# Kernel optimization log

Measured on AMD Instinct MI355X. Metric: run time of the kernel, lower is better.

Reference implementation:

```python
import jax, jax.numpy as jnp
import numpy as np

DIM = 384
HEADS = 6
HIDDEN = int(DIM * 4.0)
EPS = 1e-6

def setup_inputs() -> dict:
    key = jax.random.key(0)
    ks = jax.random.split(key, 8)
    s = 0.02
    return {
        "x": jax.random.normal(ks[0], (4, 2048, DIM), dtype=jnp.float32),
        "w_qkv": jax.random.normal(ks[1], (DIM, 3 * DIM), dtype=jnp.float32) * s,
        "b_qkv": jnp.zeros((3 * DIM,), dtype=jnp.float32),
        "w_proj": jax.random.normal(ks[2], (DIM, DIM), dtype=jnp.float32) * s,
        "b_proj": jnp.zeros((DIM,), dtype=jnp.float32),
        "w_fc1": jax.random.normal(ks[3], (DIM, HIDDEN), dtype=jnp.float32) * s,
        "b_fc1": jnp.zeros((HIDDEN,), dtype=jnp.float32),
        "w_fc2": jax.random.normal(ks[4], (HIDDEN, DIM), dtype=jnp.float32) * s,
        "b_fc2": jnp.zeros((DIM,), dtype=jnp.float32),
        "g1": jnp.ones((DIM,), dtype=jnp.float32),
        "beta1": jnp.zeros((DIM,), dtype=jnp.float32),
        "g2": jnp.ones((DIM,), dtype=jnp.float32),
        "beta2": jnp.zeros((DIM,), dtype=jnp.float32),
    }

def _layernorm(x, g, b):
    mu = jnp.mean(x, axis=-1, keepdims=True)
    var = jnp.mean(jnp.square(x - mu), axis=-1, keepdims=True)
    return (x - mu) * jax.lax.rsqrt(var + EPS) * g + b

def _attention(x, w_qkv, b_qkv, w_proj, b_proj):
    B, N, C = x.shape
    H = HEADS
    Dh = C // H
    qkv = x @ w_qkv + b_qkv                      # [B,N,3C]
    qkv = qkv.reshape(B, N, 3, H, Dh)
    q = jnp.transpose(qkv[:, :, 0], (0, 2, 1, 3))  # [B,H,N,Dh]
    k = jnp.transpose(qkv[:, :, 1], (0, 2, 1, 3))
    v = jnp.transpose(qkv[:, :, 2], (0, 2, 1, 3))
    scale = Dh ** -0.5
    attn = jnp.einsum('bhnd,bhmd->bhnm', q, k) * scale
    attn = jax.nn.softmax(attn, axis=-1)
    out = jnp.einsum('bhnm,bhmd->bhnd', attn, v)
    out = jnp.transpose(out, (0, 2, 1, 3)).reshape(B, N, C)
    return out @ w_proj + b_proj

def _mlp(x, w_fc1, b_fc1, w_fc2, b_fc2):
    h = jax.nn.gelu(x @ w_fc1 + b_fc1, approximate=False)
    return h @ w_fc2 + b_fc2

def reference(x, w_qkv, b_qkv, w_proj, b_proj, w_fc1, b_fc1, w_fc2, b_fc2, g1, beta1, g2, beta2):
    x = x + _attention(_layernorm(x, g1, beta1), w_qkv, b_qkv, w_proj, b_proj)
    x = x + _mlp(_layernorm(x, g2, beta2), w_fc1, b_fc1, w_fc2, b_fc2)
    return x
```

## Files before the change

### kernel.cpp

```cpp
#include <hip/hip_runtime.h>
#include <hip/hip_bf16.h>

#define TOK 8192
#define CDIM 384
#define HEADS 6
#define DH 64
#define HID 1536
#define SEQ 2048

#define QSCALE 0.18033688011112042f

typedef short bf16x8 __attribute__((ext_vector_type(8)));
typedef short bf16x4 __attribute__((ext_vector_type(4)));
typedef float f32x4 __attribute__((ext_vector_type(4)));
typedef void __attribute__((address_space(1))) GV;
typedef void __attribute__((address_space(3))) SV;

__device__ __forceinline__ short f2bf(float f) {
    __hip_bfloat16 h = __float2bfloat16(f);
    return *reinterpret_cast<short*>(&h);
}

__device__ __forceinline__ int pack_bf2(float a, float b) {
    __hip_bfloat162 h2 = __float22bfloat162_rn(make_float2(a, b));
    int r;
    __builtin_memcpy(&r, &h2, 4);
    return r;
}

__device__ __forceinline__ void gl_lds16(const short* g, short* lds) {
    __builtin_amdgcn_global_load_lds((GV*)g, (SV*)lds, 16, 0, 0);
}

__device__ __forceinline__ float gelu_exact(float v) {
    return 0.5f * v * (1.0f + erff(v * 0.70710678118654752f));
}

#define SWZ4(r) ((((r) & 3) ^ (((r) >> 2) & 3)))

__global__ __launch_bounds__(128) void ln_kernel(const float* __restrict__ x,
                                                 const float* __restrict__ g,
                                                 const float* __restrict__ bta,
                                                 short* __restrict__ y) {
    const int row = blockIdx.x;
    const float* xr = x + (size_t)row * CDIM;
    const int t = threadIdx.x;
    float v0 = xr[t], v1 = xr[t + 128], v2 = xr[t + 256];
    float s = v0 + v1 + v2;
    float ss = v0 * v0 + v1 * v1 + v2 * v2;
#pragma unroll
    for (int off = 1; off < 64; off <<= 1) {
        s += __shfl_xor(s, off);
        ss += __shfl_xor(ss, off);
    }
    __shared__ float sh[4];
    const int wv = t >> 6;
    if ((t & 63) == 0) { sh[wv] = s; sh[2 + wv] = ss; }
    __syncthreads();
    s = sh[0] + sh[1];
    ss = sh[2] + sh[3];
    const float mu = s * (1.0f / CDIM);
    const float var = ss * (1.0f / CDIM) - mu * mu;
    const float rs = rsqrtf(var + 1e-6f);
    short* yr = y + (size_t)row * CDIM;
    yr[t]       = f2bf((v0 - mu) * rs * g[t]       + bta[t]);
    yr[t + 128] = f2bf((v1 - mu) * rs * g[t + 128] + bta[t + 128]);
    yr[t + 256] = f2bf((v2 - mu) * rs * g[t + 256] + bta[t + 256]);
}

__global__ __launch_bounds__(256) void transpose_bf16(const float* __restrict__ w,
                                                      short* __restrict__ wT,
                                                      int K, int N) {
    __shared__ float t[32][33];
    const int bx = blockIdx.x * 32, by = blockIdx.y * 32;
    const int tx = threadIdx.x & 31, ty = threadIdx.x >> 5;
#pragma unroll
    for (int i = 0; i < 4; ++i)
        t[ty + i * 8][tx] = w[(size_t)(by + ty + i * 8) * N + bx + tx];
    __syncthreads();
#pragma unroll
    for (int i = 0; i < 4; ++i)
        wT[(size_t)(bx + ty + i * 8) * K + by + tx] = f2bf(t[tx][ty + i * 8]);
}

template <int MODE, int MT>
__global__ __launch_bounds__(256) void mfma_gemm(const short* __restrict__ A,
                                                 const short* __restrict__ WT,
                                                 const float* __restrict__ bias,
                                                 const float* __restrict__ resid,
                                                 float* __restrict__ outF,
                                                 short* __restrict__ outB,
                                                 short* __restrict__ qb,
                                                 short* __restrict__ kb,
                                                 short* __restrict__ vtb,
                                                 int M, int N, int K) {
    constexpr int BN = (MT == 4) ? 128 : 64;
    __shared__ __align__(16) short As[128 * 32];
    __shared__ __align__(16) short Bs[BN * 32];

    const int tid  = threadIdx.x;
    const int w    = tid >> 6;
    const int lane = tid & 63;
    const int quad = lane >> 4;
    const int n15  = lane & 15;
    const int wr   = (MT == 4) ? (w >> 1) : w;
    const int wc   = (MT == 4) ? (w & 1) : 0;
    const int m0   = blockIdx.y * 128;
    const int n0   = blockIdx.x * BN;

    f32x4 acc[MT][4];
#pragma unroll
    for (int i = 0; i < MT; ++i)
#pragma unroll
        for (int j = 0; j < 4; ++j) {
            acc[i][j][0] = 0; acc[i][j][1] = 0; acc[i][j][2] = 0; acc[i][j][3] = 0;
        }

    const int ca0 = tid, ca1 = tid + 256;
    const int swz = SWZ4(n15);

    for (int k0 = 0; k0 < K; k0 += 32) {
        __syncthreads();
        gl_lds16(A  + (size_t)(m0 + (ca0 >> 2)) * K + k0 + (((ca0 & 3) ^ SWZ4(ca0 >> 2)) * 8), As + w * 512);
        gl_lds16(A  + (size_t)(m0 + (ca1 >> 2)) * K + k0 + (((ca1 & 3) ^ SWZ4(ca1 >> 2)) * 8), As + 2048 + w * 512);
        gl_lds16(WT + (size_t)(n0 + (ca0 >> 2)) * K + k0 + (((ca0 & 3) ^ SWZ4(ca0 >> 2)) * 8), Bs + w * 512);
        if (MT == 4)
            gl_lds16(WT + (size_t)(n0 + (ca1 >> 2)) * K + k0 + (((ca1 & 3) ^ SWZ4(ca1 >> 2)) * 8), Bs + 2048 + w * 512);
        __syncthreads();

        bf16x8 af[MT], bfr[4];
#pragma unroll
        for (int mt = 0; mt < MT; ++mt)
            af[mt] = *(const bf16x8*)&As[(wr * (MT * 16) + mt * 16 + n15) * 32 + ((quad ^ swz) * 8)];
#pragma unroll
        for (int nt = 0; nt < 4; ++nt)
            bfr[nt] = *(const bf16x8*)&Bs[(wc * 64 + nt * 16 + n15) * 32 + ((quad ^ swz) * 8)];
#pragma unroll
        for (int mt = 0; mt < MT; ++mt)
#pragma unroll
            for (int nt = 0; nt < 4; ++nt)
                acc[mt][nt] = __builtin_amdgcn_mfma_f32_16x16x32_bf16(af[mt], bfr[nt], acc[mt][nt], 0, 0, 0);
    }

#pragma unroll
    for (int nt = 0; nt < 4; ++nt) {
        const int col = n0 + wc * 64 + nt * 16 + n15;
        const float bv = bias[col];
        if constexpr (MODE == 2) {
            const int part = col / CDIM;
            const int rem  = col - part * CDIM;
            const int h    = rem >> 6;
            const int d    = rem & 63;
#pragma unroll
            for (int mt = 0; mt < MT; ++mt)
#pragma unroll
                for (int rr = 0; rr < 4; ++rr) {
                    const int r  = m0 + wr * (MT * 16) + mt * 16 + quad * 4 + rr;
                    const int bi = r >> 11;
                    const int n  = r & 2047;
                    float o = acc[mt][nt][rr] + bv;
                    if (part == 0) o *= QSCALE;
                    const short v = f2bf(o);
                    if (part == 0)
                        qb[((size_t)(bi * HEADS + h) * SEQ + n) * DH + d] = v;
                    else if (part == 1)
                        kb[((size_t)(bi * HEADS + h) * SEQ + n) * DH + d] = v;
                    else
                        vtb[((size_t)(bi * HEADS + h) * DH + d) * SEQ + n] = v;
                }
        } else {
#pragma unroll
            for (int mt = 0; mt < MT; ++mt)
#pragma unroll
                for (int rr = 0; rr < 4; ++rr) {
                    const int r = m0 + wr * (MT * 16) + mt * 16 + quad * 4 + rr;
                    float o = acc[mt][nt][rr] + bv;
                    if constexpr (MODE == 1) {
                        outB[(size_t)r * N + col] = f2bf(gelu_exact(o));
                    } else {
                        if (resid) o += resid[(size_t)r * N + col];
                        outF[(size_t)r * N + col] = o;
                    }
                }
        }
    }
}

__global__ __launch_bounds__(256) void attn_mfma(const short* __restrict__ qb,
                                                 const short* __restrict__ kb,
                                                 const short* __restrict__ vtb,
                                                 short* __restrict__ outp) {
    __shared__ __align__(16) short Ql[64 * 64];
    __shared__ __align__(16) short Kl[64 * 64];
    __shared__ __align__(16) short Vtl[64 * 64];

    const int qt = blockIdx.x;
    const int bh = blockIdx.z * HEADS + blockIdx.y;

    const int tid  = threadIdx.x;
    const int w    = tid >> 6;
    const int lane = tid & 63;
    const int quad = lane >> 4;
    const int n15  = lane & 15;
    const int swz  = n15 & 7;

    const size_t headoff = (size_t)bh * SEQ * DH;

    {
        const short* qg = qb + headoff + (size_t)qt * 64 * DH;
#pragma unroll
        for (int i = 0; i < 2; ++i) {
            const int c = (w * 2 + i) * 64 + lane;
            const int r = c >> 3, p = c & 7;
            gl_lds16(qg + r * 64 + ((p ^ (r & 7)) * 8), Ql + (c - lane) * 8);
        }
    }

    const short* kptr[2];
    const short* vptr[2];
#pragma unroll
    for (int i = 0; i < 2; ++i) {
        const int c = (w * 2 + i) * 64 + lane;
        const int r = c >> 3, p = c & 7;
        kptr[i] = kb + headoff + r * 64 + ((p ^ (r & 7)) * 8);
        vptr[i] = vtb + (size_t)bh * DH * SEQ + (size_t)r * SEQ + ((p ^ (r & 7)) * 8);
    }

    f32x4 O[4];
    float lacc = 0.0f;
#pragma unroll
    for (int nt = 0; nt < 4; ++nt) { O[nt][0] = 0; O[nt][1] = 0; O[nt][2] = 0; O[nt][3] = 0; }

    bf16x8 qf[2];

    for (int kt = 0; kt < SEQ / 64; ++kt) {
        __syncthreads();
#pragma unroll
        for (int i = 0; i < 2; ++i) {
            gl_lds16(kptr[i], Kl + ((w * 2 + i) * 64) * 8);
            gl_lds16(vptr[i], Vtl + ((w * 2 + i) * 64) * 8);
            kptr[i] += 64 * DH;
            vptr[i] += 64;
        }
        __syncthreads();

        if (kt == 0) {
            qf[0] = *(const bf16x8*)&Ql[(w * 16 + n15) * 64 + ((quad ^ swz) * 8)];
            qf[1] = *(const bf16x8*)&Ql[(w * 16 + n15) * 64 + (((4 + quad) ^ swz) * 8)];
        }

        f32x4 S[4];
#pragma unroll
        for (int nt = 0; nt < 4; ++nt) {
            S[nt][0] = 0; S[nt][1] = 0; S[nt][2] = 0; S[nt][3] = 0;
#pragma unroll
            for (int kc = 0; kc < 2; ++kc) {
                const bf16x8 kf = *(const bf16x8*)&Kl[(nt * 16 + n15) * 64 + (((kc * 4 + quad) ^ swz) * 8)];
                S[nt] = __builtin_amdgcn_mfma_f32_16x16x32_bf16(kf, qf[kc], S[nt], 0, 0, 0);
            }
        }

        bf16x4 af16[4];
#pragma unroll
        for (int nt = 0; nt < 4; ++nt) {
            float p0 = exp2f(S[nt][0]), p1 = exp2f(S[nt][1]);
            float p2 = exp2f(S[nt][2]), p3 = exp2f(S[nt][3]);
            lacc += (p0 + p1) + (p2 + p3);
            int pk[2];
            pk[0] = pack_bf2(p0, p1);
            pk[1] = pack_bf2(p2, p3);
            __builtin_memcpy(&af16[nt], pk, 8);
        }

#pragma unroll
        for (int kc16 = 0; kc16 < 4; ++kc16) {
#pragma unroll
            for (int ntd = 0; ntd < 4; ++ntd) {
                const int row = ntd * 16 + n15;
                const int pchunk = (2 * kc16 + (quad >> 1)) ^ swz;
                const bf16x4 vf = *(const bf16x4*)&Vtl[row * 64 + pchunk * 8 + (quad & 1) * 4];
                O[ntd] = __builtin_amdgcn_mfma_f32_16x16x16bf16_1k(af16[kc16], vf, O[ntd], 0, 0, 0);
            }
        }
    }

    lacc += __shfl_xor(lacc, 16);
    lacc += __shfl_xor(lacc, 32);
    const float invq = 1.0f / lacc;
#pragma unroll
    for (int rr = 0; rr < 4; ++rr) {
        const float inv = __shfl(invq, quad * 4 + rr);
        const int row = qt * 64 + w * 16 + quad * 4 + rr;
#pragma unroll
        for (int nt = 0; nt < 4; ++nt)
            outp[(size_t)(blockIdx.z * SEQ + row) * CDIM + blockIdx.y * DH + nt * 16 + n15] =
                f2bf(O[nt][rr] * inv);
    }
}

extern "C" void kernel_launch(void* const* d_in, const int* in_sizes, int n_in,
                              void* d_out, int out_size, void* d_ws, size_t ws_size,
                              hipStream_t stream) {
    const float* x      = (const float*)d_in[0];
    const float* w_qkv  = (const float*)d_in[1];
    const float* b_qkv  = (const float*)d_in[2];
    const float* w_proj = (const float*)d_in[3];
    const float* b_proj = (const float*)d_in[4];
    const float* w_fc1  = (const float*)d_in[5];
    const float* b_fc1  = (const float*)d_in[6];
    const float* w_fc2  = (const float*)d_in[7];
    const float* b_fc2  = (const float*)d_in[8];
    const float* g1     = (const float*)d_in[9];
    const float* beta1  = (const float*)d_in[10];
    const float* g2     = (const float*)d_in[11];
    const float* beta2  = (const float*)d_in[12];
    float* out = (float*)d_out;

    short* qkvT = (short*)d_ws;
    short* projT = qkvT + 1152 * 384;
    short* fc1T  = projT + 384 * 384;
    short* fc2T  = fc1T + 1536 * 384;
    short* y     = fc2T + 384 * 1536;
    short* qb    = y + (size_t)TOK * 384;
    short* kb    = qb + (size_t)TOK * 384;
    short* vtb   = kb + (size_t)TOK * 384;
    short* attn  = vtb + (size_t)TOK * 384;
    short* hbuf  = attn + (size_t)TOK * 384;

    transpose_bf16<<<dim3(1152 / 32, 384 / 32), 256, 0, stream>>>(w_qkv, qkvT, CDIM, 3 * CDIM);
    transpose_bf16<<<dim3(384 / 32, 384 / 32), 256, 0, stream>>>(w_proj, projT, CDIM, CDIM);
    transpose_bf16<<<dim3(1536 / 32, 384 / 32), 256, 0, stream>>>(w_fc1, fc1T, CDIM, HID);
    transpose_bf16<<<dim3(384 / 32, 1536 / 32), 256, 0, stream>>>(w_fc2, fc2T, HID, CDIM);

    ln_kernel<<<TOK, 128, 0, stream>>>(x, g1, beta1, y);
    mfma_gemm<2, 4><<<dim3(1152 / 128, TOK / 128), 256, 0, stream>>>(
        y, qkvT, b_qkv, nullptr, nullptr, nullptr, qb, kb, vtb, TOK, 3 * CDIM, CDIM);
    attn_mfma<<<dim3(SEQ / 64, HEADS, 4), 256, 0, stream>>>(qb, kb, vtb, attn);
    mfma_gemm<0, 2><<<dim3(CDIM / 64, TOK / 128), 256, 0, stream>>>(
        attn, projT, b_proj, x, out, nullptr, nullptr, nullptr, nullptr, TOK, CDIM, CDIM);
    ln_kernel<<<TOK, 128, 0, stream>>>(out, g2, beta2, y);
    mfma_gemm<1, 4><<<dim3(HID / 128, TOK / 128), 256, 0, stream>>>(
        y, fc1T, b_fc1, nullptr, nullptr, hbuf, nullptr, nullptr, nullptr, TOK, HID, CDIM);
    mfma_gemm<0, 2><<<dim3(CDIM / 64, TOK / 128), 256, 0, stream>>>(
        hbuf, fc2T, b_fc2, out, out, nullptr, nullptr, nullptr, nullptr, TOK, CDIM, HID);
}
```

Baseline: 275.9 us.

## Double GEMM K-tile to 64 with 8-way swizzle, merge weight transposes, vectorize V stores

The MFMA GEMM now stages 64-wide K tiles in LDS instead of 32, with an XOR swizzle over 8 chunks. This halves the number of barrier pairs per K loop and issues more MFMAs per sync, at the cost of doubled LDS use per block. The four weight-transpose launches are merged into a single kernel that selects the matrix from the block index, saving launch overhead. The QKV epilogue writes the transposed V as packed short4 stores and hoists index math out of the per-row loop.

Result: faster. 255.5 us (-7.4%).

```diff
diff --git a/kernel.cpp b/kernel.cpp
--- a/kernel.cpp
+++ b/kernel.cpp
@@ -35,8 +35,6 @@
 __device__ __forceinline__ float gelu_exact(float v) {
     return 0.5f * v * (1.0f + erff(v * 0.70710678118654752f));
 }
-
-#define SWZ4(r) ((((r) & 3) ^ (((r) >> 2) & 3)))
 
 __global__ __launch_bounds__(128) void ln_kernel(const float* __restrict__ x,
                                                  const float* __restrict__ g,
@@ -68,11 +66,22 @@
     yr[t + 256] = f2bf((v2 - mu) * rs * g[t + 256] + bta[t + 256]);
 }
 
-__global__ __launch_bounds__(256) void transpose_bf16(const float* __restrict__ w,
-                                                      short* __restrict__ wT,
-                                                      int K, int N) {
+__global__ __launch_bounds__(256) void transpose_all(const float* __restrict__ w_qkv,
+                                                     const float* __restrict__ w_proj,
+                                                     const float* __restrict__ w_fc1,
+                                                     const float* __restrict__ w_fc2,
+                                                     short* __restrict__ qkvT,
+                                                     short* __restrict__ projT,
+                                                     short* __restrict__ fc1T,
+                                                     short* __restrict__ fc2T) {
+    int b = blockIdx.x;
+    const float* w; short* o; int K, N, nb;
+    if (b < 432)       { w = w_qkv;  o = qkvT;  K = 384;  N = 1152; nb = 36; }
+    else if (b < 576)  { b -= 432;  w = w_proj; o = projT; K = 384;  N = 384;  nb = 12; }
+    else if (b < 1152) { b -= 576;  w = w_fc1;  o = fc1T;  K = 384;  N = 1536; nb = 48; }
+    else               { b -= 1152; w = w_fc2;  o = fc2T;  K = 1536; N = 384;  nb = 12; }
+    const int bx = (b % nb) * 32, by = (b / nb) * 32;
     __shared__ float t[32][33];
-    const int bx = blockIdx.x * 32, by = blockIdx.y * 32;
     const int tx = threadIdx.x & 31, ty = threadIdx.x >> 5;
 #pragma unroll
     for (int i = 0; i < 4; ++i)
@@ -80,7 +89,7 @@
     __syncthreads();
 #pragma unroll
     for (int i = 0; i < 4; ++i)
-        wT[(size_t)(bx + ty + i * 8) * K + by + tx] = f2bf(t[tx][ty + i * 8]);
+        o[(size_t)(bx + ty + i * 8) * K + by + tx] = f2bf(t[tx][ty + i * 8]);
 }
 
 template <int MODE, int MT>
@@ -95,8 +104,8 @@
                                                  short* __restrict__ vtb,
                                                  int M, int N, int K) {
     constexpr int BN = (MT == 4) ? 128 : 64;
-    __shared__ __align__(16) short As[128 * 32];
-    __shared__ __align__(16) short Bs[BN * 32];
+    __shared__ __align__(16) short As[128 * 64];
+    __shared__ __align__(16) short Bs[BN * 64];
 
     const int tid  = threadIdx.x;
     const int w    = tid >> 6;
@@ -107,6 +116,7 @@
     const int wc   = (MT == 4) ? (w & 1) : 0;
     const int m0   = blockIdx.y * 128;
     const int n0   = blockIdx.x * BN;
+    const int swz  = n15 & 7;
 
     f32x4 acc[MT][4];
 #pragma unroll
@@ -116,30 +126,41 @@
             acc[i][j][0] = 0; acc[i][j][1] = 0; acc[i][j][2] = 0; acc[i][j][3] = 0;
         }
 
-    const int ca0 = tid, ca1 = tid + 256;
-    const int swz = SWZ4(n15);
-
-    for (int k0 = 0; k0 < K; k0 += 32) {
+    for (int k0 = 0; k0 < K; k0 += 64) {
         __syncthreads();
-        gl_lds16(A  + (size_t)(m0 + (ca0 >> 2)) * K + k0 + (((ca0 & 3) ^ SWZ4(ca0 >> 2)) * 8), As + w * 512);
-        gl_lds16(A  + (size_t)(m0 + (ca1 >> 2)) * K + k0 + (((ca1 & 3) ^ SWZ4(ca1 >> 2)) * 8), As + 2048 + w * 512);
-        gl_lds16(WT + (size_t)(n0 + (ca0 >> 2)) * K + k0 + (((ca0 & 3) ^ SWZ4(ca0 >> 2)) * 8), Bs + w * 512);
-        if (MT == 4)
-            gl_lds16(WT + (size_t)(n0 + (ca1 >> 2)) * K + k0 + (((ca1 & 3) ^ SWZ4(ca1 >> 2)) * 8), Bs + 2048 + w * 512);
+#pragma unroll
+        for (int i = 0; i < 4; ++i) {
+            const int c = i * 256 + tid;
+            const int r = c >> 3, p = c & 7;
+            gl_lds16(A + (size_t)(m0 + r) * K + k0 + ((p ^ (r & 7)) * 8),
+                     As + (i * 256 + w * 64) * 8);
+        }
+#pragma unroll
+        for (int i = 0; i < BN / 32; ++i) {
+            const int c = i * 256 + tid;
+            const int r = c >> 3, p = c & 7;
+            gl_lds16(WT + (size_t)(n0 + r) * K + k0 + ((p ^ (r & 7)) * 8),
+                     Bs + (i * 256 + w * 64) * 8);
+        }
         __syncthreads();
 
-        bf16x8 af[MT], bfr[4];
-#pragma unroll
-        for (int mt = 0; mt < MT; ++mt)
-            af[mt] = *(const bf16x8*)&As[(wr * (MT * 16) + mt * 16 + n15) * 32 + ((quad ^ swz) * 8)];
-#pragma unroll
-        for (int nt = 0; nt < 4; ++nt)
-            bfr[nt] = *(const bf16x8*)&Bs[(wc * 64 + nt * 16 + n15) * 32 + ((quad ^ swz) * 8)];
-#pragma unroll
-        for (int mt = 0; mt < MT; ++mt)
+#pragma unroll
+        for (int kk = 0; kk < 2; ++kk) {
+            bf16x8 af[MT], bfr[4];
+#pragma unroll
+            for (int mt = 0; mt < MT; ++mt)
+                af[mt] = *(const bf16x8*)&As[(wr * (MT * 16) + mt * 16 + n15) * 64 +
+                                             (((kk * 4 + quad) ^ swz) * 8)];
 #pragma unroll
             for (int nt = 0; nt < 4; ++nt)
-                acc[mt][nt] = __builtin_amdgcn_mfma_f32_16x16x32_bf16(af[mt], bfr[nt], acc[mt][nt], 0, 0, 0);
+                bfr[nt] = *(const bf16x8*)&Bs[(wc * 64 + nt * 16 + n15) * 64 +
+                                              (((kk * 4 + quad) ^ swz) * 8)];
+#pragma unroll
+            for (int mt = 0; mt < MT; ++mt)
+#pragma unroll
+                for (int nt = 0; nt < 4; ++nt)
+                    acc[mt][nt] = __builtin_amdgcn_mfma_f32_16x16x32_bf16(af[mt], bfr[nt], acc[mt][nt], 0, 0, 0);
+        }
     }
 
 #pragma unroll
@@ -152,22 +173,28 @@
             const int h    = rem >> 6;
             const int d    = rem & 63;
 #pragma unroll
-            for (int mt = 0; mt < MT; ++mt)
-#pragma unroll
-                for (int rr = 0; rr < 4; ++rr) {
-                    const int r  = m0 + wr * (MT * 16) + mt * 16 + quad * 4 + rr;
-                    const int bi = r >> 11;
-                    const int n  = r & 2047;
-                    float o = acc[mt][nt][rr] + bv;
-                    if (part == 0) o *= QSCALE;
-                    const short v = f2bf(o);
-                    if (part == 0)
-                        qb[((size_t)(bi * HEADS + h) * SEQ + n) * DH + d] = v;
-                    else if (part == 1)
-                        kb[((size_t)(bi * HEADS + h) * SEQ + n) * DH + d] = v;
-                    else
-                        vtb[((size_t)(bi * HEADS + h) * DH + d) * SEQ + n] = v;
+            for (int mt = 0; mt < MT; ++mt) {
+                const int r0 = m0 + wr * (MT * 16) + mt * 16 + quad * 4;
+                const int bi = r0 >> 11;
+                const int n  = r0 & 2047;
+                if (part == 2) {
+                    short4 pkv;
+                    pkv.x = f2bf(acc[mt][nt][0] + bv);
+                    pkv.y = f2bf(acc[mt][nt][1] + bv);
+                    pkv.z = f2bf(acc[mt][nt][2] + bv);
+                    pkv.w = f2bf(acc[mt][nt][3] + bv);
+                    *(short4*)&vtb[((size_t)(bi * HEADS + h) * DH + d) * SEQ + n] = pkv;
+                } else {
+                    short* dst = (part == 0 ? qb : kb) +
+                                 ((size_t)(bi * HEADS + h) * SEQ + n) * DH + d;
+#pragma unroll
+                    for (int rr = 0; rr < 4; ++rr) {
+                        float o = acc[mt][nt][rr] + bv;
+                        if (part == 0) o *= QSCALE;
+                        dst[(size_t)rr * DH] = f2bf(o);
+                    }
                 }
+            }
         } else {
 #pragma unroll
             for (int mt = 0; mt < MT; ++mt)
@@ -327,10 +354,8 @@
     short* attn  = vtb + (size_t)TOK * 384;
     short* hbuf  = attn + (size_t)TOK * 384;
 
-    transpose_bf16<<<dim3(1152 / 32, 384 / 32), 256, 0, stream>>>(w_qkv, qkvT, CDIM, 3 * CDIM);
-    transpose_bf16<<<dim3(384 / 32, 384 / 32), 256, 0, stream>>>(w_proj, projT, CDIM, CDIM);
-    transpose_bf16<<<dim3(1536 / 32, 384 / 32), 256, 0, stream>>>(w_fc1, fc1T, CDIM, HID);
-    transpose_bf16<<<dim3(384 / 32, 1536 / 32), 256, 0, stream>>>(w_fc2, fc2T, HID, CDIM);
+    transpose_all<<<1728, 256, 0, stream>>>(w_qkv, w_proj, w_fc1, w_fc2,
+                                            qkvT, projT, fc1T, fc2T);
 
     ln_kernel<<<TOK, 128, 0, stream>>>(x, g1, beta1, y);
     mfma_gemm<2, 4><<<dim3(1152 / 128, TOK / 128), 256, 0, stream>>>(
```
